# Kernel optimization log

Hardware: AMD Instinct MI355X
Metric: run time of the kernel (lower is better)

Reference implementation:

```python
import jax, jax.numpy as jnp
import numpy as np
import math

B, S, D, H = 8, 1024, 1024, 16
HD = D // H  # head_features = 64
SCALE = math.sqrt(HD)


def setup_inputs() -> dict:
    key = jax.random.key(0)
    k0, k1, k2, k3, k4 = jax.random.split(key, 5)
    x = jax.random.normal(k0, (B, S, D), dtype=jnp.float32)
    attn_mask = (jax.random.uniform(k1, (B, S, S)) < 0.9).astype(jnp.float32)
    w_scale = 1.0 / math.sqrt(D)  # keep unsafe exp in finite range
    Wq = jax.random.normal(k2, (D, D), dtype=jnp.float32) * w_scale
    Wk = jax.random.normal(k3, (D, D), dtype=jnp.float32) * w_scale
    Wv = jax.random.normal(k4, (D, D), dtype=jnp.float32) * w_scale
    return {"x": x, "attn_mask": attn_mask, "Wq": Wq, "Wk": Wk, "Wv": Wv}


def reference(x, attn_mask, Wq, Wk, Wv):
    b, s, _ = x.shape

    def split_heads(t):  # [b,s,D] -> [b,H,s,HD]
        return t.reshape(b, s, H, HD).transpose(0, 2, 1, 3)

    q = split_heads(x @ Wq)
    k = split_heads(x @ Wk)
    v = split_heads(x @ Wv)

    # unsafe softmax: exp without max subtraction, multiplicative mask, +1e-8 denom
    scores = jnp.einsum('bhsd,bhtd->bhst', q, k) / SCALE
    e = jnp.exp(scores) * attn_mask[:, None, :, :]
    w = e / (e.sum(axis=3, keepdims=True) + 1e-8)

    ctx = jnp.einsum('bhst,bhtd->bhsd', w, v)  # [b,H,s,HD]
    return ctx.transpose(0, 2, 1, 3).reshape(b, s, D)
```

## Files before the change

### kernel.cpp

```cpp
#include <hip/hip_runtime.h>

#define KDIM 1024

typedef _Float16 half8 __attribute__((ext_vector_type(8)));
typedef _Float16 half4 __attribute__((ext_vector_type(4)));
typedef __fp16 fp16x2 __attribute__((ext_vector_type(2)));
typedef __fp16 fp16x4 __attribute__((ext_vector_type(4)));
typedef float f32x4 __attribute__((ext_vector_type(4)));

#if defined(__has_builtin)
#if __has_builtin(__builtin_amdgcn_global_load_lds)
#define HAVE_GLDS 1
#endif
#if __has_builtin(__builtin_amdgcn_exp2f)
#define EXP2(x) __builtin_amdgcn_exp2f(x)
#endif
#if __has_builtin(__builtin_amdgcn_cvt_pkrtz)
#define HAVE_PKRTZ 1
#endif
#if __has_builtin(__builtin_amdgcn_fdot2)
#define HAVE_FDOT2 1
#endif
#endif
#ifndef EXP2
#define EXP2(x) exp2f(x)
#endif

__device__ __forceinline__ void stage16(const _Float16* g, _Float16* wave_base, int lane) {
#ifdef HAVE_GLDS
  __builtin_amdgcn_global_load_lds(
      (const __attribute__((address_space(1))) void*)g,
      (__attribute__((address_space(3))) void*)wave_base, 16, 0, 0);
#else
  *(half8*)(wave_base + lane * 8) = *(const half8*)g;
#endif
}

#define BARRIER() __builtin_amdgcn_s_barrier()

__global__ void prep_kernel(const float* __restrict__ x, const float* __restrict__ am,
                            const float* __restrict__ Wq, const float* __restrict__ Wk,
                            const float* __restrict__ Wv, _Float16* __restrict__ xb,
                            _Float16* __restrict__ Wqkvt, unsigned long long* __restrict__ bits) {
  __shared__ _Float16 tile[32][33];
  int bid = blockIdx.x;
  if (bid < 8192) {
    size_t i = ((size_t)bid * 256 + threadIdx.x) * 4;
    float4 v = *(const float4*)(x + i);
    half4 h = { (_Float16)v.x, (_Float16)v.y, (_Float16)v.z, (_Float16)v.w };
    *(half4*)(xb + i) = h;
  } else if (bid < 11264) {
    int zz = bid - 8192;
    int z = zz >> 10;
    int rem = zz & 1023;
    int bx = rem & 31, by = rem >> 5;
    const float* src = z == 0 ? Wq : (z == 1 ? Wk : Wv);
    _Float16* dst = Wqkvt + (size_t)z * KDIM * KDIM;
    float sc = (z == 0) ? 0.18033688011112042f : 1.0f;
    int tx = threadIdx.x & 31, ty = threadIdx.x >> 5;
    int c0 = bx * 32, r0 = by * 32;
#pragma unroll
    for (int i = 0; i < 4; i++) {
      int r = r0 + ty + i * 8;
      tile[tx][ty + i * 8] = (_Float16)(src[(size_t)r * KDIM + c0 + tx] * sc);
    }
    __syncthreads();
#pragma unroll
    for (int i = 0; i < 4; i++) {
      int n = c0 + ty + i * 8;
      dst[(size_t)n * KDIM + r0 + tx] = tile[ty + i * 8][tx];
    }
  } else {
    size_t i = (size_t)(bid - 11264) * 256 + threadIdx.x;
    unsigned long long b = __ballot(am[i] != 0.0f);
    if ((threadIdx.x & 63) == 0) bits[i >> 6] = b;
  }
}

__global__ __launch_bounds__(512, 4)
void gemm_kernel(const _Float16* __restrict__ A, const _Float16* __restrict__ Bt,
                 _Float16* __restrict__ Qt, _Float16* __restrict__ Kh,
                 _Float16* __restrict__ Vth) {
  __shared__ _Float16 As[2 * 8192];
  __shared__ _Float16 Bs[2 * 6144];
  int tid = threadIdx.x;
  int lane = tid & 63, w = tid >> 6;
  int la = lane & 15, qd = lane >> 4;
  int wm = w & 1, wn = w >> 1;
  int bid = blockIdx.x;
  int wg = (bid & 7) * 64 + (bid >> 3);
  int by = wg >> 4, bx = wg & 15;
  int m0 = by * 256, n0 = bx * 192;

  int srow = lane >> 2;
  int slc = ((lane & 3) ^ ((lane >> 3) & 3)) << 3;
  const _Float16* Ab = A + (size_t)m0 * KDIM;
  const _Float16* Bb = Bt + (size_t)n0 * KDIM;
  const _Float16* pAa = Ab + (size_t)(w * 16 + srow) * KDIM + slc;
  const _Float16* pAb = Ab + (size_t)(128 + w * 16 + srow) * KDIM + slc;
  const _Float16* pBa = Bb + (size_t)(w * 16 + srow) * KDIM + slc;
  const _Float16* pBb = Bb + (size_t)(128 + w * 16 + srow) * KDIM + slc;

  _Float16* ldsA0 = As + w * 512;
  _Float16* ldsA1 = As + 4096 + w * 512;
  _Float16* ldsB0 = Bs + w * 512;
  _Float16* ldsB1 = Bs + 4096 + w * 512;

  const int rc = ((qd ^ ((la >> 1) & 3)) << 3);
  const _Float16* baseA = As + (wm * 64 + la) * 32 + rc;
  const _Float16* baseB = Bs + (wn * 16 + la) * 32 + rc;

  f32x4 acc[8][3] = {};
  half8 bf[3];

#define STAGE_AB(B)                                            \
  do {                                                         \
    stage16(pAa, ldsA0 + (B) * 8192, lane);                    \
    stage16(pAb, ldsA1 + (B) * 8192, lane);                    \
    stage16(pBa, ldsB0 + (B) * 6144, lane);                    \
    if (w < 4) stage16(pBb, ldsB1 + (B) * 6144, lane);         \
    pAa += 32; pAb += 32; pBa += 32; pBb += 32;                \
  } while (0)

#define TILE(T, CUR, NXT)                                                       \
  do {                                                                          \
    if ((T) < 31) STAGE_AB(NXT);                                                \
    _Pragma("unroll") for (int nj = 0; nj < 3; ++nj)                            \
        bf[nj] = *(const half8*)(baseB + (CUR) * 6144 + nj * 2048);             \
    __builtin_amdgcn_s_setprio(1);                                              \
    _Pragma("unroll") for (int a = 0; a < 8; ++a) {                             \
      half8 afa = *(const half8*)(baseA + (CUR) * 8192 + (a >> 2) * 4096 +      \
                                  (a & 3) * 512);                               \
      _Pragma("unroll") for (int nj = 0; nj < 3; ++nj)                          \
          acc[a][nj] = __builtin_amdgcn_mfma_f32_16x16x32_f16(                  \
              afa, bf[nj], acc[a][nj], 0, 0, 0);                                \
    }                                                                           \
    __builtin_amdgcn_s_setprio(0);                                              \
    __syncthreads();                                                            \
  } while (0)

  STAGE_AB(0);
  __syncthreads();

#pragma unroll 1
  for (int tp = 0; tp < 16; ++tp) {
    TILE(2 * tp, 0, 1);
    TILE(2 * tp + 1, 1, 0);
  }

#undef TILE
#undef STAGE_AB

  int rr = lane >> 2, c4 = lane & 3;
  _Float16* ep = As + w * 1280;
#pragma unroll
  for (int mh = 0; mh < 2; ++mh) {
    int srow0 = m0 + mh * 128 + wm * 64;
    int b = srow0 >> 10, s0 = srow0 & 1023;
#pragma unroll
    for (int nj = 0; nj < 3; ++nj) {
      int colh = n0 + wn * 16 + nj * 64;
      int whichf = colh >> 10;
      int cm = colh & 1023;
      int hh = cm >> 6, d0 = cm & 63;
      if (whichf == 1) {
        _Float16* kb = Kh + (size_t)(b * 16 + hh) * 1024 * 64;
#pragma unroll
        for (int mi = 0; mi < 4; ++mi) {
          f32x4 v = acc[mh * 4 + mi][nj];
          int s = s0 + mi * 16 + qd * 4;
#pragma unroll
          for (int rg = 0; rg < 4; ++rg)
            kb[(size_t)(s + rg) * 64 + d0 + la] = (_Float16)v[rg];
        }
      } else {
        _Float16* dst = (whichf == 0) ? Qt : Vth;
#pragma unroll
        for (int mi = 0; mi < 4; ++mi) {
          f32x4 v = acc[mh * 4 + mi][nj];
          half4 hv = { (_Float16)v[0], (_Float16)v[1], (_Float16)v[2], (_Float16)v[3] };
          *(half4*)(ep + la * 72 + mi * 16 + qd * 4) = hv;
        }
        half8 o0 = *(const half8*)(ep + rr * 72 + c4 * 16);
        half8 o1 = *(const half8*)(ep + rr * 72 + c4 * 16 + 8);
        _Float16* gp = dst + ((size_t)(b * 16 + hh) * 64 + d0 + rr) * 1024 + s0 + c4 * 16;
        *(half8*)gp = o0;
        *(half8*)(gp + 8) = o1;
      }
    }
  }
}

__global__ __launch_bounds__(512, 2)
void attn_kernel(const _Float16* __restrict__ Qt, const _Float16* __restrict__ K,
                 const _Float16* __restrict__ Vt, const unsigned long long* __restrict__ mbits,
                 float* __restrict__ out) {
  __shared__ _Float16 Ks[4][2 * 64 * 32];
  __shared__ _Float16 Vs[4][2 * 64 * 40];
  __shared__ _Float16 lut16[16][4];
  int tid = threadIdx.x;
  int lane = tid & 63, w4 = tid >> 6;
  int la = lane & 15, qd = lane >> 4;
  if (tid < 64) lut16[tid >> 2][tid & 3] = (_Float16)(float)(((tid >> 2) >> (tid & 3)) & 1);
  int linear = blockIdx.x;
  int xlo = linear & 7;
  int tmp = linear >> 3;
  int qt = tmp & 3;
  int hb = (tmp >> 2) * 8 + xlo;
  int h = hb & 15, b = hb >> 4;
  const _Float16* Qp = Qt + (size_t)hb * 64 * 1024;
  const _Float16* Kp = K + (size_t)hb * 1024 * 64;
  const _Float16* Vp = Vt + (size_t)hb * 64 * 1024;
  int q0w = qt * 256 + w4 * 16;
  half8 qf[2][2];
#pragma unroll
  for (int qi = 0; qi < 2; qi++)
#pragma unroll
    for (int ks = 0; ks < 2; ks++)
#pragma unroll
      for (int j = 0; j < 8; j++)
        qf[qi][ks][j] = Qp[(size_t)(ks * 32 + qd * 8 + j) * 1024 + q0w + qi * 128 + la];
  unsigned long long mq[2][4];
#pragma unroll
  for (int qi = 0; qi < 2; qi++) {
    const ulonglong2* mp =
        (const ulonglong2*)(mbits + ((size_t)b * 1024 + q0w + qi * 128 + la) * 16 + qd * 4);
    ulonglong2 m01 = mp[0];
    ulonglong2 m23 = mp[1];
    mq[qi][0] = m01.x; mq[qi][1] = m01.y; mq[qi][2] = m23.x; mq[qi][3] = m23.y;
  }
  f32x4 acco[2][4] = {};
  float rs[2] = {0.f, 0.f};
  int kt_t = (tid & 255) >> 2;
  int kt_d = (tid >> 8) * 32 + (((tid & 3) ^ ((tid >> 2) & 3) ^ ((tid >> 4) & 3)) << 3);
  int kc8 = ((qd ^ (la & 3) ^ (la >> 2)) << 3);
  int vd = tid >> 3;
  int vt = (tid & 7) * 8;
  int vs_off = (vt >= 32 ? 2560 : 0) + vd * 40 + (vt & 31);
#if defined(HAVE_FDOT2) && defined(HAVE_PKRTZ)
  fp16x2 one2 = { (__fp16)1.0f, (__fp16)1.0f };
#endif
  {
    half8 vv0 = *(const half8*)(Vp + (size_t)vd * 1024 + vt);
    half8 vv1 = *(const half8*)(Vp + (size_t)vd * 1024 + 64 + vt);
    __builtin_amdgcn_sched_barrier(0);
    stage16(Kp + (size_t)kt_t * 64 + kt_d, Ks[0] + w4 * 512, lane);
    stage16(Kp + (size_t)(64 + kt_t) * 64 + kt_d, Ks[1] + w4 * 512, lane);
    *(half8*)(Vs[0] + vs_off) = vv0;
    *(half8*)(Vs[1] + vs_off) = vv1;
  }
  asm volatile("s_waitcnt vmcnt(0) lgkmcnt(0)" ::: "memory");
  BARRIER();

  auto compute_tile = [&](int tt) {
    const _Float16* ks_ = Ks[tt & 3];
    const _Float16* vs_ = Vs[tt & 3];
    unsigned long long mw0 = __shfl(mq[0][tt & 3], ((tt >> 2) << 4) + la);
    unsigned long long mw1 = __shfl(mq[1][tt & 3], ((tt >> 2) << 4) + la);
    unsigned long long mq0s = mw0 >> (qd * 4);
    unsigned long long mq1s = mw1 >> (qd * 4);
#pragma unroll
    for (int tsub = 0; tsub < 4; tsub++) {
      half8 kf0 = *(const half8*)(ks_ + (tsub * 16 + la) * 32 + kc8);
      half8 kf1 = *(const half8*)(ks_ + 2048 + (tsub * 16 + la) * 32 + kc8);
      f32x4 a0 = {}, a1 = {};
      __builtin_amdgcn_s_setprio(1);
      a0 = __builtin_amdgcn_mfma_f32_16x16x32_f16(kf0, qf[0][0], a0, 0, 0, 0);
      a1 = __builtin_amdgcn_mfma_f32_16x16x32_f16(kf0, qf[1][0], a1, 0, 0, 0);
      a0 = __builtin_amdgcn_mfma_f32_16x16x32_f16(kf1, qf[0][1], a0, 0, 0, 0);
      a1 = __builtin_amdgcn_mfma_f32_16x16x32_f16(kf1, qf[1][1], a1, 0, 0, 0);
      __builtin_amdgcn_s_setprio(0);
      half4 pf[2];
#pragma unroll
      for (int qi = 0; qi < 2; qi++) {
        const f32x4& aa = qi ? a1 : a0;
        unsigned nib = (unsigned)((qi ? mq1s : mq0s) >> (tsub * 16)) & 15u;
#ifdef HAVE_PKRTZ
        float e0 = EXP2(aa[0]);
        float e1 = EXP2(aa[1]);
        float e2 = EXP2(aa[2]);
        float e3 = EXP2(aa[3]);
        fp16x4 lv = *(const fp16x4*)lut16[nib];
        fp16x2 l01 = __builtin_shufflevector(lv, lv, 0, 1);
        fp16x2 l23 = __builtin_shufflevector(lv, lv, 2, 3);
        fp16x2 p01 = __builtin_amdgcn_cvt_pkrtz(e0, e1) * l01;
        fp16x2 p23 = __builtin_amdgcn_cvt_pkrtz(e2, e3) * l23;
        fp16x4 pfv = __builtin_shufflevector(p01, p23, 0, 1, 2, 3);
        pf[qi] = __builtin_bit_cast(half4, pfv);
#if defined(HAVE_FDOT2)
        rs[qi] = __builtin_amdgcn_fdot2(p01, one2, rs[qi], false);
        rs[qi] = __builtin_amdgcn_fdot2(p23, one2, rs[qi], false);
#else
        rs[qi] += (float)p01[0] + (float)p01[1] + (float)p23[0] + (float)p23[1];
#endif
#else
        float e0 = (nib & 1u) ? EXP2(aa[0]) : 0.0f;
        float e1 = (nib & 2u) ? EXP2(aa[1]) : 0.0f;
        float e2 = (nib & 4u) ? EXP2(aa[2]) : 0.0f;
        float e3 = (nib & 8u) ? EXP2(aa[3]) : 0.0f;
        pf[qi][0] = (_Float16)e0; pf[qi][1] = (_Float16)e1;
        pf[qi][2] = (_Float16)e2; pf[qi][3] = (_Float16)e3;
        rs[qi] += e0 + e1 + e2 + e3;
#endif
      }
#pragma unroll
      for (int nsub = 0; nsub < 4; nsub++) {
        half4 vf = *(const half4*)(vs_ + (tsub >> 1) * 2560 + (nsub * 16 + la) * 40 +
                                   (tsub & 1) * 16 + qd * 4);
        __builtin_amdgcn_s_setprio(1);
        acco[0][nsub] = __builtin_amdgcn_mfma_f32_16x16x16f16(pf[0], vf, acco[0][nsub], 0, 0, 0);
        acco[1][nsub] = __builtin_amdgcn_mfma_f32_16x16x16f16(pf[1], vf, acco[1][nsub], 0, 0, 0);
        __builtin_amdgcn_s_setprio(0);
      }
    }
  };

#pragma unroll
  for (int u = 0; u < 8; ++u) {
    half8 vvA, vvB;
    if (u < 7) {
      vvA = *(const half8*)(Vp + (size_t)vd * 1024 + (2 * u + 2) * 64 + vt);
      vvB = *(const half8*)(Vp + (size_t)vd * 1024 + (2 * u + 3) * 64 + vt);
      __builtin_amdgcn_sched_barrier(0);
      stage16(Kp + (size_t)((2 * u + 2) * 64 + kt_t) * 64 + kt_d,
              Ks[(2 * u + 2) & 3] + w4 * 512, lane);
      stage16(Kp + (size_t)((2 * u + 3) * 64 + kt_t) * 64 + kt_d,
              Ks[(2 * u + 3) & 3] + w4 * 512, lane);
    }
    compute_tile(2 * u);
    if (u < 7) *(half8*)(Vs[(2 * u + 2) & 3] + vs_off) = vvA;
    compute_tile(2 * u + 1);
    if (u < 7) {
      *(half8*)(Vs[(2 * u + 3) & 3] + vs_off) = vvB;
      asm volatile("s_waitcnt vmcnt(0) lgkmcnt(0)" ::: "memory");
      BARRIER();
    }
  }

  float* op = out + (size_t)b * 1024 * 1024 + (size_t)h * 64;
#pragma unroll
  for (int qi = 0; qi < 2; qi++) {
    float r0 = rs[qi];
    r0 += __shfl_xor(r0, 16);
    r0 += __shfl_xor(r0, 32);
    float inv_q = 1.0f / (r0 + 1e-8f);
#pragma unroll
    for (int rg = 0; rg < 4; rg++) {
      float inv = __shfl(inv_q, qd * 4 + rg);
      int s = q0w + qi * 128 + qd * 4 + rg;
#pragma unroll
      for (int nsub = 0; nsub < 4; nsub++)
        op[(size_t)s * 1024 + nsub * 16 + la] = acco[qi][nsub][rg] * inv;
    }
  }
}

extern "C" void kernel_launch(void* const* d_in, const int* in_sizes, int n_in,
                              void* d_out, int out_size, void* d_ws, size_t ws_size,
                              hipStream_t stream) {
  (void)in_sizes; (void)n_in; (void)out_size; (void)ws_size;
  const float* x = (const float*)d_in[0];
  const float* am = (const float*)d_in[1];
  const float* Wq = (const float*)d_in[2];
  const float* Wk = (const float*)d_in[3];
  const float* Wv = (const float*)d_in[4];
  float* out = (float*)d_out;

  char* p = (char*)d_ws;
  _Float16* xb = (_Float16*)p;    p += (size_t)8192 * 1024 * 2;
  _Float16* Wqkvt = (_Float16*)p; p += (size_t)3 * 1024 * 1024 * 2;
  _Float16* Qt = (_Float16*)p;    p += (size_t)8192 * 1024 * 2;
  _Float16* Kh = (_Float16*)p;    p += (size_t)8192 * 1024 * 2;
  _Float16* Vth = (_Float16*)p;   p += (size_t)8192 * 1024 * 2;
  unsigned long long* mb = (unsigned long long*)p;

  prep_kernel<<<44032, 256, 0, stream>>>(x, am, Wq, Wk, Wv, xb, Wqkvt, mb);
  gemm_kernel<<<dim3(512), 512, 0, stream>>>(xb, Wqkvt, Qt, Kh, Vth);
  attn_kernel<<<512, 512, 0, stream>>>(Qt, Kh, Vth, mb, out);
}
```

Baseline: 274.9 us.

## Vectorize mask bit-packing and stop unrolling the attention main loop

The mask-packing blocks in the prep kernel now read four floats per thread as a float4 and assemble each 64-bit mask word with XOR shuffles across 16 lanes. This cuts the number of mask blocks by four, and the grid shrinks from 44032 to 19456 blocks to match. In the attention kernel the 8-iteration outer loop is no longer unrolled, and LDS buffers are indexed by computed offsets so the loop body can stay rolled. The rolled loop is meant to reduce code size and register pressure, at the cost of dynamic indexing and possibly worse instruction scheduling.

```diff
diff --git a/kernel.cpp b/kernel.cpp
--- a/kernel.cpp
+++ b/kernel.cpp
@@ -71,9 +71,16 @@
       dst[(size_t)n * KDIM + r0 + tx] = tile[ty + i * 8][tx];
     }
   } else {
-    size_t i = (size_t)(bid - 11264) * 256 + threadIdx.x;
-    unsigned long long b = __ballot(am[i] != 0.0f);
-    if ((threadIdx.x & 63) == 0) bits[i >> 6] = b;
+    size_t i4 = ((size_t)(bid - 11264) * 256 + threadIdx.x) * 4;
+    float4 v = *(const float4*)(am + i4);
+    unsigned nib = (unsigned)(v.x != 0.0f) | ((unsigned)(v.y != 0.0f) << 1) |
+                   ((unsigned)(v.z != 0.0f) << 2) | ((unsigned)(v.w != 0.0f) << 3);
+    unsigned long long word = (unsigned long long)nib << ((threadIdx.x & 15) * 4);
+    word |= __shfl_xor(word, 1);
+    word |= __shfl_xor(word, 2);
+    word |= __shfl_xor(word, 4);
+    word |= __shfl_xor(word, 8);
+    if ((threadIdx.x & 15) == 0) bits[i4 >> 6] = word;
   }
 }
 
@@ -197,7 +204,7 @@
                  float* __restrict__ out) {
   __shared__ _Float16 Ks[4][2 * 64 * 32];
   __shared__ _Float16 Vs[4][2 * 64 * 40];
-  __shared__ _Float16 lut16[16][4];
+  __shared__ __align__(8) _Float16 lut16[16][4];
   int tid = threadIdx.x;
   int lane = tid & 63, w4 = tid >> 6;
   int la = lane & 15, qd = lane >> 4;
@@ -253,8 +260,8 @@
   BARRIER();
 
   auto compute_tile = [&](int tt) {
-    const _Float16* ks_ = Ks[tt & 3];
-    const _Float16* vs_ = Vs[tt & 3];
+    const _Float16* ks_ = Ks[0] + (tt & 3) * 4096;
+    const _Float16* vs_ = Vs[0] + (tt & 3) * 5120;
     unsigned long long mw0 = __shfl(mq[0][tt & 3], ((tt >> 2) << 4) + la);
     unsigned long long mw1 = __shfl(mq[1][tt & 3], ((tt >> 2) << 4) + la);
     unsigned long long mq0s = mw0 >> (qd * 4);
@@ -315,7 +322,7 @@
     }
   };
 
-#pragma unroll
+#pragma unroll 1
   for (int u = 0; u < 8; ++u) {
     half8 vvA, vvB;
     if (u < 7) {
@@ -323,15 +330,16 @@
       vvB = *(const half8*)(Vp + (size_t)vd * 1024 + (2 * u + 3) * 64 + vt);
       __builtin_amdgcn_sched_barrier(0);
       stage16(Kp + (size_t)((2 * u + 2) * 64 + kt_t) * 64 + kt_d,
-              Ks[(2 * u + 2) & 3] + w4 * 512, lane);
+              Ks[0] + ((2 * u + 2) & 3) * 4096 + w4 * 512, lane);
       stage16(Kp + (size_t)((2 * u + 3) * 64 + kt_t) * 64 + kt_d,
-              Ks[(2 * u + 3) & 3] + w4 * 512, lane);
+              Ks[0] + ((2 * u + 3) & 3) * 4096 + w4 * 512, lane);
     }
     compute_tile(2 * u);
-    if (u < 7) *(half8*)(Vs[(2 * u + 2) & 3] + vs_off) = vvA;
+    if (u < 7)
+      *(half8*)(Vs[0] + ((2 * u + 2) & 3) * 5120 + vs_off) = vvA;
     compute_tile(2 * u + 1);
     if (u < 7) {
-      *(half8*)(Vs[(2 * u + 3) & 3] + vs_off) = vvB;
+      *(half8*)(Vs[0] + ((2 * u + 3) & 3) * 5120 + vs_off) = vvB;
       asm volatile("s_waitcnt vmcnt(0) lgkmcnt(0)" ::: "memory");
       BARRIER();
     }
@@ -374,7 +382,7 @@
   _Float16* Vth = (_Float16*)p;   p += (size_t)8192 * 1024 * 2;
   unsigned long long* mb = (unsigned long long*)p;
 
-  prep_kernel<<<44032, 256, 0, stream>>>(x, am, Wq, Wk, Wv, xb, Wqkvt, mb);
+  prep_kernel<<<19456, 256, 0, stream>>>(x, am, Wq, Wk, Wv, xb, Wqkvt, mb);
   gemm_kernel<<<dim3(512), 512, 0, stream>>>(xb, Wqkvt, Qt, Kh, Vth);
   attn_kernel<<<512, 512, 0, stream>>>(Qt, Kh, Vth, mb, out);
 }
```

New measurement: 244.7 us. 11.0% less time.
